# Kernel optimization log

Measured on AMD Instinct MI355X. Metric: run time of the kernel, lower is better.

The kernel has to match this reference:

```python
import jax, jax.numpy as jnp
import numpy as np

NEG_SLOPE = 0.2

def _gatv2(x_src, x_dst, src, dst, Wl, bl, Wr, br, att, bias, num_dst, edge_feat=None, We=None):
    # PyG GATv2Conv (heads=1, add_self_loops=False, eval mode -> no dropout)
    xl = x_src @ Wl + bl                      # [Ns, C] lin_l on source
    xr = x_dst @ Wr + br                      # [Nd, C] lin_r on target
    m = xl[src] + xr[dst]                     # [E, C]
    if edge_feat is not None:
        m = m + edge_feat @ We                # lin_edge (bias=False)
    e = jax.nn.leaky_relu(m, NEG_SLOPE) @ att # [E] attention logits
    emax = jax.ops.segment_max(e, dst, num_segments=num_dst)
    ee = jnp.exp(e - emax[dst])
    denom = jax.ops.segment_sum(ee, dst, num_segments=num_dst)
    alpha = ee / jnp.maximum(denom[dst], 1e-16)
    out = jax.ops.segment_sum(alpha[:, None] * xl[src], dst, num_segments=num_dst)
    return out + bias


def setup_inputs() -> dict:
    key = jax.random.key(0)
    N_OP, N_M, N_A = 50000, 5000, 2000
    C_OP, C_M, C_A = 256, 128, 128
    E_OO, E_OM, E_MA, E_DIM = 200000, 200000, 60000, 8
    ks = jax.random.split(key, 40)
    i = iter(range(40))
    def nrm(shape, fan_in):
        return jax.random.normal(ks[next(i)], shape, dtype=jnp.float32) / np.sqrt(fan_in)
    inp = {}
    inp['x_op'] = jax.random.normal(ks[next(i)], (N_OP, C_OP), dtype=jnp.float32)
    inp['x_m'] = jax.random.normal(ks[next(i)], (N_M, C_M), dtype=jnp.float32)
    inp['x_a'] = jax.random.normal(ks[next(i)], (N_A, C_A), dtype=jnp.float32)
    inp['ei_pred'] = jax.random.randint(ks[next(i)], (2, E_OO), 0, N_OP)
    inp['ei_succ'] = jax.random.randint(ks[next(i)], (2, E_OO), 0, N_OP)
    inp['src_o2m'] = jax.random.randint(ks[next(i)], (E_OM,), 0, N_OP)
    inp['dst_o2m'] = jax.random.randint(ks[next(i)], (E_OM,), 0, N_M)
    inp['src_m2a'] = jax.random.randint(ks[next(i)], (E_MA,), 0, N_M)
    inp['dst_m2a'] = jax.random.randint(ks[next(i)], (E_MA,), 0, N_A)
    inp['ea_m2a'] = jax.random.normal(ks[next(i)], (E_MA, E_DIM), dtype=jnp.float32)
    for name, c_in_src, c_in_dst, c_out in [('pred', C_OP, C_OP, C_OP), ('succ', C_OP, C_OP, C_OP), ('o2m', C_OP, C_M, C_M), ('m2a', C_M, C_A, C_A)]:
        inp[f'Wl_{name}'] = nrm((c_in_src, c_out), c_in_src)
        inp[f'bl_{name}'] = jnp.zeros((c_out,), jnp.float32)
        inp[f'Wr_{name}'] = nrm((c_in_dst, c_out), c_in_dst)
        inp[f'br_{name}'] = jnp.zeros((c_out,), jnp.float32)
        inp[f'att_{name}'] = nrm((c_out,), c_out)
        inp[f'b_{name}'] = jnp.zeros((c_out,), jnp.float32)
    inp['We_m2a'] = nrm((E_DIM, C_A), E_DIM)
    return inp


def reference(x_op, x_m, x_a, ei_pred, ei_succ, src_o2m, dst_o2m, src_m2a, dst_m2a, ea_m2a,
              Wl_pred, bl_pred, Wr_pred, br_pred, att_pred, b_pred,
              Wl_succ, bl_succ, Wr_succ, br_succ, att_succ, b_succ,
              Wl_o2m, bl_o2m, Wr_o2m, br_o2m, att_o2m, b_o2m,
              Wl_m2a, bl_m2a, Wr_m2a, br_m2a, att_m2a, b_m2a, We_m2a):
    N_OP, N_M, N_A = x_op.shape[0], x_m.shape[0], x_a.shape[0]
    # operation_relation_extract: two op->op GATv2 convs, HeteroConv sum-aggregated
    f_pred = _gatv2(x_op, x_op, ei_pred[0], ei_pred[1], Wl_pred, bl_pred, Wr_pred, br_pred, att_pred, b_pred, N_OP)
    f_succ = _gatv2(x_op, x_op, ei_succ[0], ei_succ[1], Wl_succ, bl_succ, Wr_succ, br_succ, att_succ, b_succ, N_OP)
    # hetero_relation_extract
    f_mach = _gatv2(x_op, x_m, src_o2m, dst_o2m, Wl_o2m, bl_o2m, Wr_o2m, br_o2m, att_o2m, b_o2m, N_M)
    f_agv = _gatv2(x_m, x_a, src_m2a, dst_m2a, Wl_m2a, bl_m2a, Wr_m2a, br_m2a, att_m2a, b_m2a, N_A, edge_feat=ea_m2a, We=We_m2a)
    # residual sum across relation outputs per node type
    out_op = x_op + f_pred + f_succ
    out_m = x_m + f_mach
    out_a = x_a + f_agv
    return (out_op, out_m, out_a)
```

## Files before the change

### kernel.cpp

```cpp
#include <hip/hip_runtime.h>

#define N_OP   50000
#define N_M    5000
#define N_A    2000
#define C_OP   256
#define C_M    128
#define C_A    128
#define E_OO   200000
#define E_OM   200000
#define E_MA   60000
#define E_DIM  8

#define OUT_OP_OFF 0
#define OUT_M_OFF  (N_OP * C_OP)
#define OUT_A_OFF  (N_OP * C_OP + N_M * C_M)

typedef short bf16x8 __attribute__((ext_vector_type(8)));
typedef float f32x4 __attribute__((ext_vector_type(4)));
typedef __attribute__((address_space(1))) const unsigned gu32;
typedef __attribute__((address_space(3))) unsigned lu32;

__device__ __forceinline__ unsigned short f2bf(float f) {
    unsigned u = __float_as_uint(f);
    unsigned r = (u + 0x7FFFu + ((u >> 16) & 1u)) >> 16;
    return (unsigned short)r;
}
__device__ __forceinline__ float bf2f(unsigned short h) {
    return __uint_as_float(((unsigned)h) << 16);
}

#define NTOT 107000
#define ETOT 660000

#define I3_OP (N_OP * C_OP / 4)
#define I3_M  (I3_OP + N_M * C_M / 4)
#define I3_A  (I3_M + N_A * C_A / 4)

#define PK_P   131072
#define PK_S   262144
#define PK_OL  294912
#define PK_OR  311296
#define PK_ML  327680
#define PK_MR  344064
#define PK_BP  344576
#define PK_BS  345088

#define PREP_HIST_BLK ((ETOT + 255) / 256)
#define PREP_INIT_BLK (I3_A / 256)
#define PREP_PACK_BLK (PK_BS / 256)
#define PREP_TOTAL    17670

__device__ __forceinline__ void init_one(const float* __restrict__ x,
                                         const float* __restrict__ b1,
                                         const float* __restrict__ b2,
                                         float* __restrict__ out,
                                         unsigned short* __restrict__ xc,
                                         int i, int cmask) {
    float4 v = ((const float4*)x)[i];
    const int cb = i & cmask;
    float4 b = ((const float4*)b1)[cb];
    if (b2) {
        float4 t = ((const float4*)b2)[cb];
        b.x += t.x; b.y += t.y; b.z += t.z; b.w += t.w;
    }
    float4 o;
    o.x = v.x + b.x; o.y = v.y + b.y; o.z = v.z + b.z; o.w = v.w + b.w;
    ((float4*)out)[i] = o;
    ushort4 r;
    r.x = f2bf(v.x); r.y = f2bf(v.y); r.z = f2bf(v.z); r.w = f2bf(v.w);
    ((ushort4*)xc)[i] = r;
}

__global__ void prep_all(
    const int* __restrict__ dP, const int* __restrict__ dS,
    const int* __restrict__ dO, const int* __restrict__ dA,
    int* __restrict__ cP, int* __restrict__ cS,
    int* __restrict__ cO, int* __restrict__ cA, int* __restrict__ rk,
    const float* __restrict__ x_op, const float* __restrict__ x_m,
    const float* __restrict__ x_a,
    const float* __restrict__ bP, const float* __restrict__ bS,
    const float* __restrict__ bO, const float* __restrict__ bA,
    float* __restrict__ out_op, float* __restrict__ out_m, float* __restrict__ out_a,
    unsigned short* __restrict__ xcop, unsigned short* __restrict__ xcm,
    unsigned short* __restrict__ xca,
    const float* __restrict__ WlP, const float* __restrict__ WrP,
    const float* __restrict__ WlS, const float* __restrict__ WrS,
    const float* __restrict__ WOl, const float* __restrict__ WOr,
    const float* __restrict__ WMl, const float* __restrict__ WMr,
    const float* __restrict__ blP, const float* __restrict__ brP,
    const float* __restrict__ blS, const float* __restrict__ brS,
    unsigned short* __restrict__ BtP, unsigned short* __restrict__ BtS,
    unsigned short* __restrict__ BtOL, unsigned short* __restrict__ BtOR,
    unsigned short* __restrict__ BtML, unsigned short* __restrict__ BtMR,
    float* __restrict__ biasP, float* __restrict__ biasS) {
    const int b = blockIdx.x;
    const int tid = threadIdx.x;
    if ((b % 6) == 5) {
        const int hb = b / 6;
        if (hb >= PREP_HIST_BLK) return;
        int i = hb * 256 + tid;
        if (i < 200000)      rk[i] = atomicAdd(&cP[dP[i]], 1);
        else if (i < 400000) rk[i] = atomicAdd(&cS[dS[i - 200000]], 1);
        else if (i < 600000) rk[i] = atomicAdd(&cO[dO[i - 400000]], 1);
        else if (i < ETOT)   rk[i] = atomicAdd(&cA[dA[i - 600000]], 1);
        return;
    }
    const int ob = b - b / 6;
    if (ob < PREP_INIT_BLK) {
        int i = ob * 256 + tid;
        if (i < I3_OP)      init_one(x_op, bP, bS, out_op, xcop, i, 63);
        else if (i < I3_M)  init_one(x_m, bO, nullptr, out_m, xcm, i - I3_OP, 31);
        else                init_one(x_a, bA, nullptr, out_a, xca, i - I3_M, 31);
    } else {
        int i = (ob - PREP_INIT_BLK) * 256 + tid;
        if (i < PK_P) {
            int n = i >> 8, k = i & 255;
            BtP[i] = f2bf((n < 256) ? WlP[k * 256 + n] : WrP[k * 256 + (n - 256)]);
        } else if (i < PK_S) {
            int j = i - PK_P; int n = j >> 8, k = j & 255;
            BtS[j] = f2bf((n < 256) ? WlS[k * 256 + n] : WrS[k * 256 + (n - 256)]);
        } else if (i < PK_OL) {
            int j = i - PK_S; int n = j >> 8, k = j & 255;
            BtOL[j] = f2bf(WOl[k * 128 + n]);
        } else if (i < PK_OR) {
            int j = i - PK_OL; int n = j >> 7, k = j & 127;
            BtOR[j] = f2bf(WOr[k * 128 + n]);
        } else if (i < PK_ML) {
            int j = i - PK_OR; int n = j >> 7, k = j & 127;
            BtML[j] = f2bf(WMl[k * 128 + n]);
        } else if (i < PK_MR) {
            int j = i - PK_ML; int n = j >> 7, k = j & 127;
            BtMR[j] = f2bf(WMr[k * 128 + n]);
        } else if (i < PK_BP) {
            int j = i - PK_MR;
            biasP[j] = (j < 256) ? blP[j] : brP[j - 256];
        } else if (i < PK_BS) {
            int j = i - PK_BP;
            biasS[j] = (j < 256) ? blS[j] : brS[j - 256];
        }
    }
}

__device__ __forceinline__ void gload_lds16(const void* g, void* l) {
    __builtin_amdgcn_global_load_lds((gu32*)g, (lu32*)l, 16, 0, 0);
}

#define GEMM_IDX                                                                \
    const int tid  = threadIdx.x;                                               \
    const int lane = tid & 63;                                                  \
    const int wid  = tid >> 6;                                                  \
    const int m0   = bx * 128;                                                  \
    const int n0   = by * 128;                                                  \
    f32x4 acc[4][4] = {};                                                       \
    const int srow  = tid >> 3;                                                 \
    const int scolb = (tid & 7) * 16;                                           \
    const int scole = (scolb ^ ((srow & 7) << 4)) >> 1;                         \
    int grA[4], grB[4];                                                         \
    _Pragma("unroll")                                                           \
    for (int i = 0; i < 4; ++i) {                                               \
        int gr = m0 + i * 32 + srow;                                            \
        grA[i] = (gr < M) ? gr : M - 1;                                         \
        grB[i] = n0 + i * 32 + srow;                                            \
    }                                                                           \
    const int nt = K >> 6;

#define GEMM_COMPUTE(BUFA, BUFB)                                                \
    _Pragma("unroll")                                                           \
    for (int kh = 0; kh < 2; ++kh) {                                            \
        const int kob = kh * 64 + (lane >> 4) * 16;                             \
        bf16x8 a[4], bfr[4];                                                    \
        _Pragma("unroll")                                                       \
        for (int mi = 0; mi < 4; ++mi) {                                        \
            const int row = wr + mi * 16 + (lane & 15);                         \
            a[mi] = *(const bf16x8*)((const char*)(BUFA) + row * 128 +          \
                                     (kob ^ ((row & 7) << 4)));                 \
        }                                                                       \
        _Pragma("unroll")                                                       \
        for (int ni = 0; ni < 4; ++ni) {                                        \
            const int row = wc + ni * 16 + (lane & 15);                         \
            bfr[ni] = *(const bf16x8*)((const char*)(BUFB) + row * 128 +        \
                                       (kob ^ ((row & 7) << 4)));               \
        }                                                                       \
        _Pragma("unroll")                                                       \
        for (int mi = 0; mi < 4; ++mi)                                          \
            _Pragma("unroll")                                                   \
            for (int ni = 0; ni < 4; ++ni)                                      \
                acc[mi][ni] = __builtin_amdgcn_mfma_f32_16x16x32_bf16(          \
                    a[mi], bfr[ni], acc[mi][ni], 0, 0, 0);                      \
    }

#define GEMM_EPILOGUE                                                           \
    const int crow = (lane >> 4) * 4;                                           \
    const int ccol = lane & 15;                                                 \
    float bcol[4];                                                              \
    _Pragma("unroll")                                                           \
    for (int ni = 0; ni < 4; ++ni) bcol[ni] = bias[n0 + wc + ni * 16 + ccol];   \
    _Pragma("unroll")                                                           \
    for (int mi = 0; mi < 4; ++mi) {                                            \
        _Pragma("unroll")                                                       \
        for (int j = 0; j < 4; ++j) {                                           \
            const int row = m0 + wr + mi * 16 + crow + j;                       \
            if (row < M) {                                                      \
                unsigned short* pc = C + (size_t)row * ldc + n0 + wc + ccol;    \
                _Pragma("unroll")                                               \
                for (int ni = 0; ni < 4; ++ni)                                  \
                    pc[ni * 16] = f2bf(acc[mi][ni][j] + bcol[ni]);              \
            }                                                                   \
        }                                                                       \
    }

__device__ __forceinline__ void gemm_body(
    const unsigned short* __restrict__ A, const unsigned short* __restrict__ Bt,
    const float* __restrict__ bias, unsigned short* __restrict__ C,
    int M, int K, int ldc, int bx, int by,
    unsigned short (&As)[2][128 * 64], unsigned short (&Bs)[2][128 * 64]) {
    GEMM_IDX
    int cur = 0;
#define STAGE(buf, k0)                                                          \
    {                                                                           \
        _Pragma("unroll")                                                       \
        for (int i = 0; i < 4; ++i)                                             \
            gload_lds16(A + (size_t)grA[i] * K + (k0) + scole,                  \
                        &As[buf][i * 2048 + tid * 8]);                          \
        _Pragma("unroll")                                                       \
        for (int i = 0; i < 4; ++i)                                             \
            gload_lds16(Bt + (size_t)grB[i] * K + (k0) + scole,                 \
                        &Bs[buf][i * 2048 + tid * 8]);                          \
    }
    STAGE(0, 0)
    asm volatile("s_waitcnt vmcnt(0)" ::: "memory");
    __syncthreads();
    const int wr = (wid >> 1) * 64;
    const int wc = (wid & 1) * 64;
    for (int t = 0; t < nt; ++t) {
        if (t + 1 < nt) STAGE(cur ^ 1, (t + 1) * 64)
        GEMM_COMPUTE(As[cur], Bs[cur])
        asm volatile("s_waitcnt vmcnt(0)" ::: "memory");
        __syncthreads();
        cur ^= 1;
    }
#undef STAGE
    GEMM_EPILOGUE
}

__device__ __forceinline__ void gemm_body_sb(
    const unsigned short* __restrict__ A, const unsigned short* __restrict__ Bt,
    const float* __restrict__ bias, unsigned short* __restrict__ C,
    int M, int K, int ldc, int bx, int by,
    unsigned short (&As)[128 * 64], unsigned short (&Bs)[128 * 64]) {
    GEMM_IDX
    const int wr = (wid >> 1) * 64;
    const int wc = (wid & 1) * 64;
    for (int t = 0; t < nt; ++t) {
#pragma unroll
        for (int i = 0; i < 4; ++i)
            gload_lds16(A + (size_t)grA[i] * K + t * 64 + scole, &As[i * 2048 + tid * 8]);
#pragma unroll
        for (int i = 0; i < 4; ++i)
            gload_lds16(Bt + (size_t)grB[i] * K + t * 64 + scole, &Bs[i * 2048 + tid * 8]);
        asm volatile("s_waitcnt vmcnt(0)" ::: "memory");
        __syncthreads();
        GEMM_COMPUTE(As, Bs)
        __syncthreads();
    }
    GEMM_EPILOGUE
}

__global__ __launch_bounds__(256) void mfma_gemm(
    const unsigned short* __restrict__ A, const unsigned short* __restrict__ Bt,
    const float* __restrict__ bias, unsigned short* __restrict__ C,
    int M, int K, int ldc) {
    __shared__ unsigned short As[2][128 * 64];
    __shared__ unsigned short Bs[2][128 * 64];
    gemm_body(A, Bt, bias, C, M, K, ldc, blockIdx.x, blockIdx.y, As, Bs);
}

#define SCAT_XBLK 645
__global__ __launch_bounds__(256) void gemm_scat(
    const unsigned short* __restrict__ A, const unsigned short* __restrict__ Bt,
    const float* __restrict__ bias, unsigned short* __restrict__ C,
    int M, int K, int ldc, int mt,
    const int* __restrict__ sP, const int* __restrict__ dP,
    const int* __restrict__ sS, const int* __restrict__ dS,
    const int* __restrict__ sO, const int* __restrict__ dO,
    const int* __restrict__ sA, const int* __restrict__ dA,
    const int* __restrict__ pP, const int* __restrict__ pS,
    const int* __restrict__ pO, const int* __restrict__ pA,
    const int* __restrict__ rk,
    int* __restrict__ srP, int* __restrict__ srS,
    int* __restrict__ srO, int* __restrict__ srA, int* __restrict__ eiA) {
    __shared__ unsigned short As[2][128 * 64];
    __shared__ unsigned short Bs[2][128 * 64];
    if ((int)blockIdx.x < mt) {
        gemm_body(A, Bt, bias, C, M, K, ldc, blockIdx.x, blockIdx.y, As, Bs);
    } else {
        const int i = (((int)blockIdx.x - mt) * 4 + (int)blockIdx.y) * 256 + (int)threadIdx.x;
        if (i < 200000) {
            srP[pP[dP[i]] + rk[i]] = sP[i];
        } else if (i < 400000) {
            const int j = i - 200000;
            srS[pS[dS[j]] + rk[i]] = sS[j];
        } else if (i < 600000) {
            const int j = i - 400000;
            srO[pO[dO[j]] + rk[i]] = sO[j];
        } else if (i < ETOT) {
            const int j = i - 600000;
            const int pos = pA[dA[j]] + rk[i];
            srA[pos] = sA[j];
            eiA[pos] = j;
        }
    }
}

#define NB_P 49
#define NB_S 49
#define NB_O 5
#define NB_A 2

__global__ void zero4(int* __restrict__ p, int n) {
    int i = blockIdx.x * blockDim.x + threadIdx.x;
    if (i < n) p[i] = 0;
}

__global__ void scan_blk4(const int* __restrict__ cP, const int* __restrict__ cS,
                          const int* __restrict__ cO, const int* __restrict__ cA,
                          int* __restrict__ pP, int* __restrict__ pS,
                          int* __restrict__ pO, int* __restrict__ pA,
                          int* __restrict__ bsum) {
    __shared__ int smem[1024];
    int b = blockIdx.x;
    const int* cnt; int* ptr; int n; int bo;
    if (b < NB_P)                { cnt = cP; ptr = pP; n = 50000; bo = 0; }
    else if (b < NB_P + NB_S)    { cnt = cS; ptr = pS; n = 50000; bo = 64;  b -= NB_P; }
    else if (b < NB_P + NB_S + NB_O) { cnt = cO; ptr = pO; n = 5000; bo = 128; b -= NB_P + NB_S; }
    else                         { cnt = cA; ptr = pA; n = 2000; bo = 192; b -= NB_P + NB_S + NB_O; }
    const int tid = threadIdx.x;
    const int i = b * 1024 + tid;
    const int v = (i < n) ? cnt[i] : 0;
    smem[tid] = v;
    __syncthreads();
    for (int o = 1; o < 1024; o <<= 1) {
        int t = (tid >= o) ? smem[tid - o] : 0;
        __syncthreads();
        smem[tid] += t;
        __syncthreads();
    }
    if (i < n) ptr[i] = smem[tid] - v;
    if (tid == 1023) bsum[bo + b] = smem[1023];
}

__global__ void scan_tops4(const int* __restrict__ bsum, int* __restrict__ boff,
                           int* __restrict__ pP, int* __restrict__ pS,
                           int* __restrict__ pO, int* __restrict__ pA) {
    __shared__ int smem[1024];
    const int seg = blockIdx.x;
    const int nb = (seg < 2) ? 49 : (seg == 2 ? 5 : 2);
    const int off = seg * 64;
    int* ptr_n = (seg == 0) ? pP + 50000 : (seg == 1) ? pS + 50000
               : (seg == 2) ? pO + 5000 : pA + 2000;
    const int tid = threadIdx.x;
    const int v = (tid < nb) ? bsum[off + tid] : 0;
    smem[tid] = v;
    __syncthreads();
    for (int o = 1; o < 1024; o <<= 1) {
        int t = (tid >= o) ? smem[tid - o] : 0;
        __syncthreads();
        smem[tid] += t;
        __syncthreads();
    }
    if (tid < nb) boff[off + tid] = smem[tid] - v;
    if (tid == 1023) *ptr_n = smem[1023];
}

__global__ void scan_add4(int* __restrict__ pP, int* __restrict__ pS,
                          int* __restrict__ pO, int* __restrict__ pA,
                          const int* __restrict__ boff) {
    int i = blockIdx.x * blockDim.x + threadIdx.x;
    int* ptr; int loc; int off;
    if (i < 50000)       { ptr = pP; loc = i;          off = 0; }
    else if (i < 100000) { ptr = pS; loc = i - 50000;  off = 64; }
    else if (i < 105000) { ptr = pO; loc = i - 100000; off = 128; }
    else if (i < NTOT)   { ptr = pA; loc = i - 105000; off = 192; }
    else return;
    ptr[loc] += boff[off + (loc >> 10)];
}

__device__ __forceinline__ void csr2_body(
    const unsigned short* __restrict__ xl, int ldl,
    const unsigned short* __restrict__ xr, int ldr,
    const float* __restrict__ att,
    const int* __restrict__ ptr, const int* __restrict__ srcs,
    float* __restrict__ out, int n, int blk) {
    const int tid = threadIdx.x;
    const int node = blk * 8 + (tid >> 5);
    if (node >= n) return;
    const int gl = tid & 31;
    const int beg = ptr[node], end = ptr[node + 1];
    if (beg == end) return;

    constexpr int V = 8;
    const int c0 = gl * V;

    float av[V], rvf[V];
    {
        const unsigned short* pr = xr + (size_t)node * ldr + c0;
        unsigned short rv[V];
        *(uint4*)rv = *(const uint4*)pr;
#pragma unroll
        for (int v4 = 0; v4 < V / 4; ++v4)
            *(float4*)(av + v4 * 4) = ((const float4*)(att + c0))[v4];
#pragma unroll
        for (int v = 0; v < V; ++v) rvf[v] = bf2f(rv[v]);
    }

    float runM = -3.0e38f, runS = 0.0f;
    float acc[V] = {};

    unsigned short lv[V];
    {
        const unsigned short* pl = xl + (size_t)srcs[beg] * ldl + c0;
        *(uint4*)lv = *(const uint4*)pl;
    }

    for (int j = beg; j < end; ++j) {
        float cf[V];
#pragma unroll
        for (int v = 0; v < V; ++v) cf[v] = bf2f(lv[v]);
        if (j + 1 < end) {
            const unsigned short* pl = xl + (size_t)srcs[j + 1] * ldl + c0;
            *(uint4*)lv = *(const uint4*)pl;
        }

        float part = 0.0f;
#pragma unroll
        for (int v = 0; v < V; ++v) {
            float m = cf[v] + rvf[v];
            m = (m >= 0.0f) ? m : 0.2f * m;
            part += m * av[v];
        }
        part += __shfl_xor(part, 1, 64);
        part += __shfl_xor(part, 2, 64);
        part += __shfl_xor(part, 4, 64);
        part += __shfl_xor(part, 8, 64);
        part += __shfl_xor(part, 16, 64);

        const float newM = fmaxf(runM, part);
        const float sc = __expf(runM - newM);
        const float e1 = __expf(part - newM);
        runS = runS * sc + e1;
        runM = newM;
#pragma unroll
        for (int v = 0; v < V; ++v) acc[v] = acc[v] * sc + e1 * cf[v];
    }

    const float inv = 1.0f / fmaxf(runS, 1e-16f);
    float* po = out + (size_t)node * 256 + c0;
#pragma unroll
    for (int v4 = 0; v4 < V / 4; ++v4) {
        float4 o = ((float4*)po)[v4];
        o.x += acc[v4 * 4 + 0] * inv;
        o.y += acc[v4 * 4 + 1] * inv;
        o.z += acc[v4 * 4 + 2] * inv;
        o.w += acc[v4 * 4 + 3] * inv;
        ((float4*)po)[v4] = o;
    }
}

__global__ void csr_serial2(const unsigned short* __restrict__ xl, int ldl,
                            const unsigned short* __restrict__ xr, int ldr,
                            const float* __restrict__ att,
                            const int* __restrict__ ptr, const int* __restrict__ srcs,
                            float* __restrict__ out, int n) {
    csr2_body(xl, ldl, xr, ldr, att, ptr, srcs, out, n, blockIdx.x);
}

template <bool EF>
__device__ __forceinline__ void csrg_body(
    const unsigned short* __restrict__ xl, const unsigned short* __restrict__ xr,
    const float* __restrict__ att,
    const int* __restrict__ ptr, const int* __restrict__ srcs,
    const int* __restrict__ eid, const float* __restrict__ ea,
    const float* __restrict__ We,
    float* __restrict__ out, int n, int blk) {
    const int node = blk * 4 + ((int)threadIdx.x >> 6);
    if (node >= n) return;
    const int lane = threadIdx.x & 63;
    const int grp  = lane >> 4;
    const int sl   = lane & 15;
    const int beg = ptr[node], end = ptr[node + 1];
    if (beg == end) return;

    constexpr int W = 8;
    const int c0 = sl * W;

    float av[W], rvf[W];
    {
        const unsigned short* pr = xr + (size_t)node * 128 + c0;
        unsigned short rv[W];
        *(uint4*)rv = *(const uint4*)pr;
#pragma unroll
        for (int v4 = 0; v4 < 2; ++v4)
            *(float4*)(av + v4 * 4) = ((const float4*)(att + c0))[v4];
#pragma unroll
        for (int v = 0; v < W; ++v) rvf[v] = bf2f(rv[v]);
    }

    float wreg[64];
    if constexpr (EF) {
#pragma unroll
        for (int k = 0; k < 8; ++k) {
            *(float4*)(wreg + k * 8)     = *(const float4*)(We + k * 128 + c0);
            *(float4*)(wreg + k * 8 + 4) = *(const float4*)(We + k * 128 + c0 + 4);
        }
    }

    float runM = -3.0e38f, runS = 0.0f;
    float acc[W] = {};

    for (int cb = beg; cb < end; cb += 4) {
        const int j = cb + grp;
        const bool act = (j < end);
        const int js = act ? j : end - 1;
        const int s = srcs[js];

        const unsigned short* pl = xl + (size_t)s * 128 + c0;
        unsigned short lv[W];
        *(uint4*)lv = *(const uint4*)pl;
        float cf[W];
#pragma unroll
        for (int v = 0; v < W; ++v) cf[v] = bf2f(lv[v]);

        float part = 0.0f;
        if constexpr (EF) {
            const int oe = eid[js];
            float eav[8];
            *(float4*)eav       = *(const float4*)(ea + (size_t)oe * 8);
            *(float4*)(eav + 4) = *(const float4*)(ea + (size_t)oe * 8 + 4);
#pragma unroll
            for (int v = 0; v < W; ++v) {
                float efv = eav[0] * wreg[v];
#pragma unroll
                for (int k = 1; k < 8; ++k) efv += eav[k] * wreg[k * 8 + v];
                float m = cf[v] + rvf[v] + efv;
                m = (m >= 0.0f) ? m : 0.2f * m;
                part += m * av[v];
            }
        } else {
#pragma unroll
            for (int v = 0; v < W; ++v) {
                float m = cf[v] + rvf[v];
                m = (m >= 0.0f) ? m : 0.2f * m;
                part += m * av[v];
            }
        }
        part += __shfl_xor(part, 1, 64);
        part += __shfl_xor(part, 2, 64);
        part += __shfl_xor(part, 4, 64);
        part += __shfl_xor(part, 8, 64);
        if (!act) part = -3.0e38f;

        float cm = fmaxf(part, __shfl_xor(part, 16, 64));
        cm = fmaxf(cm, __shfl_xor(cm, 32, 64));

        if (cm > runM) {
            const float sc = __expf(runM - cm);
            runS *= sc;
#pragma unroll
            for (int v = 0; v < W; ++v) acc[v] *= sc;
            runM = cm;
        }
        const float w = act ? __expf(part - runM) : 0.0f;
        float cs = w + __shfl_xor(w, 16, 64);
        cs += __shfl_xor(cs, 32, 64);
        runS += cs;
#pragma unroll
        for (int v = 0; v < W; ++v) acc[v] += w * cf[v];
    }

#pragma unroll
    for (int v = 0; v < W; ++v) acc[v] += __shfl_xor(acc[v], 16, 64);
#pragma unroll
    for (int v = 0; v < W; ++v) acc[v] += __shfl_xor(acc[v], 32, 64);

    const float inv = 1.0f / fmaxf(runS, 1e-16f);
    if (grp == 0) {
        float* po = out + (size_t)node * 128 + c0;
#pragma unroll
        for (int v4 = 0; v4 < 2; ++v4) {
            float4 o = ((float4*)po)[v4];
            o.x += acc[v4 * 4 + 0] * inv;
            o.y += acc[v4 * 4 + 1] * inv;
            o.z += acc[v4 * 4 + 2] * inv;
            o.w += acc[v4 * 4 + 3] * inv;
            ((float4*)po)[v4] = o;
        }
    }
}

#define MT_OPB 391
#define MT_MB  40
#define MT_AB  16
#define PG_GEMM (MT_OPB + MT_MB + MT_MB + MT_AB)

__global__ __launch_bounds__(256) void fuse_pg(
    const unsigned short* __restrict__ xc_op, const unsigned short* __restrict__ xc_m,
    const unsigned short* __restrict__ xc_a,
    const unsigned short* __restrict__ BtOL, const unsigned short* __restrict__ BtOR,
    const unsigned short* __restrict__ BtML, const unsigned short* __restrict__ BtMR,
    const float* __restrict__ blO, const float* __restrict__ brO,
    const float* __restrict__ blM, const float* __restrict__ brM,
    unsigned short* __restrict__ xlbO, unsigned short* __restrict__ xrbO,
    unsigned short* __restrict__ xlbM, unsigned short* __restrict__ xrbM,
    const unsigned short* __restrict__ H, const float* __restrict__ attP,
    const int* __restrict__ ptrP, const int* __restrict__ srcP,
    float* __restrict__ out_op) {
    __shared__ unsigned short As[128 * 64];
    __shared__ unsigned short Bs[128 * 64];
    const int b = blockIdx.x;
    if (b < MT_OPB) {
        gemm_body_sb(xc_op, BtOL, blO, xlbO, N_OP, 256, 128, b, 0, As, Bs);
    } else if (b < MT_OPB + MT_MB) {
        gemm_body_sb(xc_m, BtOR, brO, xrbO, N_M, 128, 128, b - MT_OPB, 0, As, Bs);
    } else if (b < MT_OPB + 2 * MT_MB) {
        gemm_body_sb(xc_m, BtML, blM, xlbM, N_M, 128, 128, b - MT_OPB - MT_MB, 0, As, Bs);
    } else if (b < PG_GEMM) {
        gemm_body_sb(xc_a, BtMR, brM, xrbM, N_A, 128, 128, b - MT_OPB - 2 * MT_MB, 0, As, Bs);
    } else {
        csr2_body(H, 512, H + 256, 512, attP, ptrP, srcP, out_op, N_OP, b - PG_GEMM);
    }
}

#define CP_O 1250
__global__ void csr_pair(
    const unsigned short* __restrict__ xlbO, const unsigned short* __restrict__ xrbO,
    const float* __restrict__ attO,
    const int* __restrict__ ptrO, const int* __restrict__ srcO,
    float* __restrict__ out_m,
    const unsigned short* __restrict__ xlbM, const unsigned short* __restrict__ xrbM,
    const float* __restrict__ attA,
    const int* __restrict__ ptrA, const int* __restrict__ srcA,
    const int* __restrict__ eidA, const float* __restrict__ ea,
    const float* __restrict__ We, float* __restrict__ out_a) {
    const int b = blockIdx.x;
    if (b < CP_O)
        csrg_body<false>(xlbO, xrbO, attO, ptrO, srcO, nullptr, nullptr, nullptr,
                         out_m, N_M, b);
    else
        csrg_body<true>(xlbM, xrbM, attA, ptrA, srcA, eidA, ea, We,
                        out_a, N_A, b - CP_O);
}

#define F_H      0
#define F_XCOP   12800000
#define F_XCM    19200000
#define F_XCA    19520000
#define F_BTP    19648000
#define F_BTS    19713536
#define F_BTOL   19779072
#define F_BTOR   19795456
#define F_BTML   19803648
#define F_BTMR   19811840
#define F_BIASP  19820032
#define F_BIASS  19820544
#define F_CNT4   19821056
#define F_BSUM   19928056
#define F_BOFF   19928312
#define F_PTR_P  19928568
#define F_SRC_P  19978569
#define F_PTR_S  20178569
#define F_SRC_S  20228570
#define F_PTR_O  20428570
#define F_SRC_O  20433571
#define F_PTR_A  20633571
#define F_SRC_A  20635572
#define F_EID_A  20695572
#define F_RANK   20755572
#define F_XLO    21415572
#define F_XRO    24615572
#define F_XLM    24935572
#define F_XRM    25255572

extern "C" void kernel_launch(void* const* d_in, const int* in_sizes, int n_in,
                              void* d_out, int out_size, void* d_ws, size_t ws_size,
                              hipStream_t stream) {
    const float* x_op    = (const float*)d_in[0];
    const float* x_m     = (const float*)d_in[1];
    const float* x_a     = (const float*)d_in[2];
    const int*   ei_pred = (const int*)d_in[3];
    const int*   ei_succ = (const int*)d_in[4];
    const int*   src_o2m = (const int*)d_in[5];
    const int*   dst_o2m = (const int*)d_in[6];
    const int*   src_m2a = (const int*)d_in[7];
    const int*   dst_m2a = (const int*)d_in[8];
    const float* ea_m2a  = (const float*)d_in[9];

    const float* Wl_pred = (const float*)d_in[10];
    const float* bl_pred = (const float*)d_in[11];
    const float* Wr_pred = (const float*)d_in[12];
    const float* br_pred = (const float*)d_in[13];
    const float* att_pred= (const float*)d_in[14];
    const float* b_pred  = (const float*)d_in[15];

    const float* Wl_succ = (const float*)d_in[16];
    const float* bl_succ = (const float*)d_in[17];
    const float* Wr_succ = (const float*)d_in[18];
    const float* br_succ = (const float*)d_in[19];
    const float* att_succ= (const float*)d_in[20];
    const float* b_succ  = (const float*)d_in[21];

    const float* Wl_o2m  = (const float*)d_in[22];
    const float* bl_o2m  = (const float*)d_in[23];
    const float* Wr_o2m  = (const float*)d_in[24];
    const float* br_o2m  = (const float*)d_in[25];
    const float* att_o2m = (const float*)d_in[26];
    const float* b_o2m   = (const float*)d_in[27];

    const float* Wl_m2a  = (const float*)d_in[28];
    const float* bl_m2a  = (const float*)d_in[29];
    const float* Wr_m2a  = (const float*)d_in[30];
    const float* br_m2a  = (const float*)d_in[31];
    const float* att_m2a = (const float*)d_in[32];
    const float* b_m2a   = (const float*)d_in[33];
    const float* We_m2a  = (const float*)d_in[34];

    float* ws = (float*)d_ws;
    unsigned short* H     = (unsigned short*)(ws + F_H);
    unsigned short* xc_op = (unsigned short*)(ws + F_XCOP);
    unsigned short* xc_m  = (unsigned short*)(ws + F_XCM);
    unsigned short* xc_a  = (unsigned short*)(ws + F_XCA);
    unsigned short* BtP   = (unsigned short*)(ws + F_BTP);
    unsigned short* BtS   = (unsigned short*)(ws + F_BTS);
    unsigned short* BtOL  = (unsigned short*)(ws + F_BTOL);
    unsigned short* BtOR  = (unsigned short*)(ws + F_BTOR);
    unsigned short* BtML  = (unsigned short*)(ws + F_BTML);
    unsigned short* BtMR  = (unsigned short*)(ws + F_BTMR);
    float* biasP = ws + F_BIASP;
    float* biasS = ws + F_BIASS;
    int* cntP = (int*)(ws + F_CNT4);
    int* cntS = cntP + 50000;
    int* cntO = cntP + 100000;
    int* cntA = cntP + 105000;
    int* bsum = (int*)(ws + F_BSUM);
    int* boff = (int*)(ws + F_BOFF);
    int* ptrP = (int*)(ws + F_PTR_P); int* srcP = (int*)(ws + F_SRC_P);
    int* ptrS = (int*)(ws + F_PTR_S); int* srcS = (int*)(ws + F_SRC_S);
    int* ptrO = (int*)(ws + F_PTR_O); int* srcO = (int*)(ws + F_SRC_O);
    int* ptrA = (int*)(ws + F_PTR_A); int* srcA = (int*)(ws + F_SRC_A);
    int* eidA = (int*)(ws + F_EID_A);
    int* rk   = (int*)(ws + F_RANK);
    unsigned short* xlbO = (unsigned short*)(ws + F_XLO);
    unsigned short* xrbO = (unsigned short*)(ws + F_XRO);
    unsigned short* xlbM = (unsigned short*)(ws + F_XLM);
    unsigned short* xrbM = (unsigned short*)(ws + F_XRM);

    float* out_op = (float*)d_out + OUT_OP_OFF;
    float* out_m  = (float*)d_out + OUT_M_OFF;
    float* out_a  = (float*)d_out + OUT_A_OFF;

    zero4<<<(NTOT + 255) / 256, 256, 0, stream>>>(cntP, NTOT);

    prep_all<<<PREP_TOTAL, 256, 0, stream>>>(
        ei_pred + E_OO, ei_succ + E_OO, dst_o2m, dst_m2a,
        cntP, cntS, cntO, cntA, rk,
        x_op, x_m, x_a, b_pred, b_succ, b_o2m, b_m2a,
        out_op, out_m, out_a, xc_op, xc_m, xc_a,
        Wl_pred, Wr_pred, Wl_succ, Wr_succ, Wl_o2m, Wr_o2m, Wl_m2a, Wr_m2a,
        bl_pred, br_pred, bl_succ, br_succ,
        BtP, BtS, BtOL, BtOR, BtML, BtMR, biasP, biasS);

    scan_blk4<<<NB_P + NB_S + NB_O + NB_A, 1024, 0, stream>>>(cntP, cntS, cntO, cntA,
                                                              ptrP, ptrS, ptrO, ptrA, bsum);
    scan_tops4<<<4, 1024, 0, stream>>>(bsum, boff, ptrP, ptrS, ptrO, ptrA);
    scan_add4<<<(NTOT + 255) / 256, 256, 0, stream>>>(ptrP, ptrS, ptrO, ptrA, boff);

    gemm_scat<<<dim3(MT_OPB + SCAT_XBLK, 4), 256, 0, stream>>>(
        xc_op, BtP, biasP, H, N_OP, 256, 512, MT_OPB,
        ei_pred, ei_pred + E_OO, ei_succ, ei_succ + E_OO,
        src_o2m, dst_o2m, src_m2a, dst_m2a,
        ptrP, ptrS, ptrO, ptrA, rk,
        srcP, srcS, srcO, srcA, eidA);

    fuse_pg<<<PG_GEMM + (N_OP + 7) / 8, 256, 0, stream>>>(
        xc_op, xc_m, xc_a, BtOL, BtOR, BtML, BtMR,
        bl_o2m, br_o2m, bl_m2a, br_m2a,
        xlbO, xrbO, xlbM, xrbM,
        H, att_pred, ptrP, srcP, out_op);

    mfma_gemm<<<dim3(MT_OPB, 4), 256, 0, stream>>>(xc_op, BtS, biasS, H, N_OP, 256, 512);

    csr_serial2<<<(N_OP + 7) / 8, 256, 0, stream>>>(H, 512, H + 256, 512,
                                                    att_succ, ptrS, srcS, out_op, N_OP);

    csr_pair<<<CP_O + (N_A + 3) / 4, 256, 0, stream>>>(
        xlbO, xrbO, att_o2m, ptrO, srcO, out_m,
        xlbM, xrbM, att_m2a, ptrA, srcA, eidA, ea_m2a, We_m2a, out_a);
}
```

Baseline: 311.6 us.

## Move small o2m/m2a GEMMs into the pred GEMM+scatter launch

The four small projection GEMMs (o2m lin_l/lin_r, m2a lin_l/lin_r) move out of the fused kernel that also ran the pred CSR aggregation and into the first GEMM+scatter launch. They now use the double-buffered GEMM body instead of the single-buffered one, and the pred aggregation runs as its own csr_serial2 launch. The aim is to overlap the small GEMMs with the large pred GEMM and the CSR scatter, and to give them the pipelined load path. The trade-off is that the pred aggregation no longer overlaps with those GEMMs, and the first kernel now needs double-buffered LDS for every block.

Result: faster. 271.6 us (-12.8%).

```diff
diff --git a/kernel.cpp b/kernel.cpp
--- a/kernel.cpp
+++ b/kernel.cpp
@@ -145,77 +145,34 @@
     __builtin_amdgcn_global_load_lds((gu32*)g, (lu32*)l, 16, 0, 0);
 }
 
-#define GEMM_IDX                                                                \
-    const int tid  = threadIdx.x;                                               \
-    const int lane = tid & 63;                                                  \
-    const int wid  = tid >> 6;                                                  \
-    const int m0   = bx * 128;                                                  \
-    const int n0   = by * 128;                                                  \
-    f32x4 acc[4][4] = {};                                                       \
-    const int srow  = tid >> 3;                                                 \
-    const int scolb = (tid & 7) * 16;                                           \
-    const int scole = (scolb ^ ((srow & 7) << 4)) >> 1;                         \
-    int grA[4], grB[4];                                                         \
-    _Pragma("unroll")                                                           \
-    for (int i = 0; i < 4; ++i) {                                               \
-        int gr = m0 + i * 32 + srow;                                            \
-        grA[i] = (gr < M) ? gr : M - 1;                                         \
-        grB[i] = n0 + i * 32 + srow;                                            \
-    }                                                                           \
-    const int nt = K >> 6;
-
-#define GEMM_COMPUTE(BUFA, BUFB)                                                \
-    _Pragma("unroll")                                                           \
-    for (int kh = 0; kh < 2; ++kh) {                                            \
-        const int kob = kh * 64 + (lane >> 4) * 16;                             \
-        bf16x8 a[4], bfr[4];                                                    \
-        _Pragma("unroll")                                                       \
-        for (int mi = 0; mi < 4; ++mi) {                                        \
-            const int row = wr + mi * 16 + (lane & 15);                         \
-            a[mi] = *(const bf16x8*)((const char*)(BUFA) + row * 128 +          \
-                                     (kob ^ ((row & 7) << 4)));                 \
-        }                                                                       \
-        _Pragma("unroll")                                                       \
-        for (int ni = 0; ni < 4; ++ni) {                                        \
-            const int row = wc + ni * 16 + (lane & 15);                         \
-            bfr[ni] = *(const bf16x8*)((const char*)(BUFB) + row * 128 +        \
-                                       (kob ^ ((row & 7) << 4)));               \
-        }                                                                       \
-        _Pragma("unroll")                                                       \
-        for (int mi = 0; mi < 4; ++mi)                                          \
-            _Pragma("unroll")                                                   \
-            for (int ni = 0; ni < 4; ++ni)                                      \
-                acc[mi][ni] = __builtin_amdgcn_mfma_f32_16x16x32_bf16(          \
-                    a[mi], bfr[ni], acc[mi][ni], 0, 0, 0);                      \
-    }
-
-#define GEMM_EPILOGUE                                                           \
-    const int crow = (lane >> 4) * 4;                                           \
-    const int ccol = lane & 15;                                                 \
-    float bcol[4];                                                              \
-    _Pragma("unroll")                                                           \
-    for (int ni = 0; ni < 4; ++ni) bcol[ni] = bias[n0 + wc + ni * 16 + ccol];   \
-    _Pragma("unroll")                                                           \
-    for (int mi = 0; mi < 4; ++mi) {                                            \
-        _Pragma("unroll")                                                       \
-        for (int j = 0; j < 4; ++j) {                                           \
-            const int row = m0 + wr + mi * 16 + crow + j;                       \
-            if (row < M) {                                                      \
-                unsigned short* pc = C + (size_t)row * ldc + n0 + wc + ccol;    \
-                _Pragma("unroll")                                               \
-                for (int ni = 0; ni < 4; ++ni)                                  \
-                    pc[ni * 16] = f2bf(acc[mi][ni][j] + bcol[ni]);              \
-            }                                                                   \
-        }                                                                       \
-    }
-
 __device__ __forceinline__ void gemm_body(
     const unsigned short* __restrict__ A, const unsigned short* __restrict__ Bt,
     const float* __restrict__ bias, unsigned short* __restrict__ C,
     int M, int K, int ldc, int bx, int by,
     unsigned short (&As)[2][128 * 64], unsigned short (&Bs)[2][128 * 64]) {
-    GEMM_IDX
+    const int tid  = threadIdx.x;
+    const int lane = tid & 63;
+    const int wid  = tid >> 6;
+    const int m0   = bx * 128;
+    const int n0   = by * 128;
+
+    f32x4 acc[4][4] = {};
+
+    const int srow   = tid >> 3;
+    const int scolb  = (tid & 7) * 16;
+    const int scole  = (scolb ^ ((srow & 7) << 4)) >> 1;
+
+    int grA[4], grB[4];
+#pragma unroll
+    for (int i = 0; i < 4; ++i) {
+        int gr = m0 + i * 32 + srow;
+        grA[i] = (gr < M) ? gr : M - 1;
+        grB[i] = n0 + i * 32 + srow;
+    }
+
+    const int nt = K >> 6;
     int cur = 0;
+
 #define STAGE(buf, k0)                                                          \
     {                                                                           \
         _Pragma("unroll")                                                       \
@@ -227,43 +184,63 @@
             gload_lds16(Bt + (size_t)grB[i] * K + (k0) + scole,                 \
                         &Bs[buf][i * 2048 + tid * 8]);                          \
     }
+
     STAGE(0, 0)
     asm volatile("s_waitcnt vmcnt(0)" ::: "memory");
     __syncthreads();
+
     const int wr = (wid >> 1) * 64;
     const int wc = (wid & 1) * 64;
+
     for (int t = 0; t < nt; ++t) {
         if (t + 1 < nt) STAGE(cur ^ 1, (t + 1) * 64)
-        GEMM_COMPUTE(As[cur], Bs[cur])
+#pragma unroll
+        for (int kh = 0; kh < 2; ++kh) {
+            const int kob = kh * 64 + (lane >> 4) * 16;
+            bf16x8 a[4], b[4];
+#pragma unroll
+            for (int mi = 0; mi < 4; ++mi) {
+                const int row = wr + mi * 16 + (lane & 15);
+                a[mi] = *(const bf16x8*)((const char*)As[cur] + row * 128 +
+                                         (kob ^ ((row & 7) << 4)));
+            }
+#pragma unroll
+            for (int ni = 0; ni < 4; ++ni) {
+                const int row = wc + ni * 16 + (lane & 15);
+                b[ni] = *(const bf16x8*)((const char*)Bs[cur] + row * 128 +
+                                         (kob ^ ((row & 7) << 4)));
+            }
+#pragma unroll
+            for (int mi = 0; mi < 4; ++mi)
+#pragma unroll
+                for (int ni = 0; ni < 4; ++ni)
+                    acc[mi][ni] = __builtin_amdgcn_mfma_f32_16x16x32_bf16(
+                        a[mi], b[ni], acc[mi][ni], 0, 0, 0);
+        }
         asm volatile("s_waitcnt vmcnt(0)" ::: "memory");
         __syncthreads();
         cur ^= 1;
     }
 #undef STAGE
-    GEMM_EPILOGUE
-}
-
-__device__ __forceinline__ void gemm_body_sb(
-    const unsigned short* __restrict__ A, const unsigned short* __restrict__ Bt,
-    const float* __restrict__ bias, unsigned short* __restrict__ C,
-    int M, int K, int ldc, int bx, int by,
-    unsigned short (&As)[128 * 64], unsigned short (&Bs)[128 * 64]) {
-    GEMM_IDX
-    const int wr = (wid >> 1) * 64;
-    const int wc = (wid & 1) * 64;
-    for (int t = 0; t < nt; ++t) {
-#pragma unroll
-        for (int i = 0; i < 4; ++i)
-            gload_lds16(A + (size_t)grA[i] * K + t * 64 + scole, &As[i * 2048 + tid * 8]);
-#pragma unroll
-        for (int i = 0; i < 4; ++i)
-            gload_lds16(Bt + (size_t)grB[i] * K + t * 64 + scole, &Bs[i * 2048 + tid * 8]);
-        asm volatile("s_waitcnt vmcnt(0)" ::: "memory");
-        __syncthreads();
-        GEMM_COMPUTE(As, Bs)
-        __syncthreads();
-    }
-    GEMM_EPILOGUE
+
+    const int crow = (lane >> 4) * 4;
+    const int ccol = lane & 15;
+    float bcol[4];
+#pragma unroll
+    for (int ni = 0; ni < 4; ++ni) bcol[ni] = bias[n0 + wc + ni * 16 + ccol];
+#pragma unroll
+    for (int mi = 0; mi < 4; ++mi) {
+#pragma unroll
+        for (int j = 0; j < 4; ++j) {
+            const int row = m0 + wr + mi * 16 + crow + j;
+            if (row < M) {
+                unsigned short* pc = C + (size_t)row * ldc + n0 + wc + ccol;
+#pragma unroll
+                for (int ni = 0; ni < 4; ++ni)
+                    pc[ni * 16] = f2bf(acc[mi][ni][j] + bcol[ni]);
+            }
+        }
+    }
 }
 
 __global__ __launch_bounds__(256) void mfma_gemm(
@@ -275,11 +252,24 @@
     gemm_body(A, Bt, bias, C, M, K, ldc, blockIdx.x, blockIdx.y, As, Bs);
 }
 
+#define MT_OPB 391
+#define MT_MB  40
+#define MT_AB  16
+#define SMALL_G (MT_OPB + MT_MB + MT_MB + MT_AB)
+#define SMALL_XBLK 122
 #define SCAT_XBLK 645
-__global__ __launch_bounds__(256) void gemm_scat(
-    const unsigned short* __restrict__ A, const unsigned short* __restrict__ Bt,
-    const float* __restrict__ bias, unsigned short* __restrict__ C,
-    int M, int K, int ldc, int mt,
+
+__global__ __launch_bounds__(256) void gemm_multi(
+    const unsigned short* __restrict__ xc_op, const unsigned short* __restrict__ xc_m,
+    const unsigned short* __restrict__ xc_a,
+    const unsigned short* __restrict__ BtP, const float* __restrict__ biasP,
+    unsigned short* __restrict__ H,
+    const unsigned short* __restrict__ BtOL, const unsigned short* __restrict__ BtOR,
+    const unsigned short* __restrict__ BtML, const unsigned short* __restrict__ BtMR,
+    const float* __restrict__ blO, const float* __restrict__ brO,
+    const float* __restrict__ blM, const float* __restrict__ brM,
+    unsigned short* __restrict__ xlbO, unsigned short* __restrict__ xrbO,
+    unsigned short* __restrict__ xlbM, unsigned short* __restrict__ xrbM,
     const int* __restrict__ sP, const int* __restrict__ dP,
     const int* __restrict__ sS, const int* __restrict__ dS,
     const int* __restrict__ sO, const int* __restrict__ dO,
@@ -291,10 +281,21 @@
     int* __restrict__ srO, int* __restrict__ srA, int* __restrict__ eiA) {
     __shared__ unsigned short As[2][128 * 64];
     __shared__ unsigned short Bs[2][128 * 64];
-    if ((int)blockIdx.x < mt) {
-        gemm_body(A, Bt, bias, C, M, K, ldc, blockIdx.x, blockIdx.y, As, Bs);
+    const int bx = blockIdx.x, by = blockIdx.y;
+    if (bx < MT_OPB) {
+        gemm_body(xc_op, BtP, biasP, H, N_OP, 256, 512, bx, by, As, Bs);
+    } else if (bx < MT_OPB + SMALL_XBLK) {
+        const int idx = (bx - MT_OPB) * 4 + by;
+        if (idx < MT_OPB)
+            gemm_body(xc_op, BtOL, blO, xlbO, N_OP, 256, 128, idx, 0, As, Bs);
+        else if (idx < MT_OPB + MT_MB)
+            gemm_body(xc_m, BtOR, brO, xrbO, N_M, 128, 128, idx - MT_OPB, 0, As, Bs);
+        else if (idx < MT_OPB + 2 * MT_MB)
+            gemm_body(xc_m, BtML, blM, xlbM, N_M, 128, 128, idx - MT_OPB - MT_MB, 0, As, Bs);
+        else if (idx < SMALL_G)
+            gemm_body(xc_a, BtMR, brM, xrbM, N_A, 128, 128, idx - MT_OPB - 2 * MT_MB, 0, As, Bs);
     } else {
-        const int i = (((int)blockIdx.x - mt) * 4 + (int)blockIdx.y) * 256 + (int)threadIdx.x;
+        const int i = ((bx - MT_OPB - SMALL_XBLK) * 4 + by) * 256 + (int)threadIdx.x;
         if (i < 200000) {
             srP[pP[dP[i]] + rk[i]] = sP[i];
         } else if (i < 400000) {
@@ -385,14 +386,13 @@
     ptr[loc] += boff[off + (loc >> 10)];
 }
 
-__device__ __forceinline__ void csr2_body(
-    const unsigned short* __restrict__ xl, int ldl,
-    const unsigned short* __restrict__ xr, int ldr,
-    const float* __restrict__ att,
-    const int* __restrict__ ptr, const int* __restrict__ srcs,
-    float* __restrict__ out, int n, int blk) {
+__global__ void csr_serial2(const unsigned short* __restrict__ xl, int ldl,
+                            const unsigned short* __restrict__ xr, int ldr,
+                            const float* __restrict__ att,
+                            const int* __restrict__ ptr, const int* __restrict__ srcs,
+                            float* __restrict__ out, int n) {
     const int tid = threadIdx.x;
-    const int node = blk * 8 + (tid >> 5);
+    const int node = blockIdx.x * 8 + (tid >> 5);
     if (node >= n) return;
     const int gl = tid & 31;
     const int beg = ptr[node], end = ptr[node + 1];
@@ -464,14 +464,6 @@
         o.w += acc[v4 * 4 + 3] * inv;
         ((float4*)po)[v4] = o;
     }
-}
-
-__global__ void csr_serial2(const unsigned short* __restrict__ xl, int ldl,
-                            const unsigned short* __restrict__ xr, int ldr,
-                            const float* __restrict__ att,
-                            const int* __restrict__ ptr, const int* __restrict__ srcs,
-                            float* __restrict__ out, int n) {
-    csr2_body(xl, ldl, xr, ldr, att, ptr, srcs, out, n, blockIdx.x);
 }
 
 template <bool EF>
@@ -594,39 +586,6 @@
             o.w += acc[v4 * 4 + 3] * inv;
             ((float4*)po)[v4] = o;
         }
-    }
-}
-
-#define MT_OPB 391
-#define MT_MB  40
-#define MT_AB  16
-#define PG_GEMM (MT_OPB + MT_MB + MT_MB + MT_AB)
-
-__global__ __launch_bounds__(256) void fuse_pg(
-    const unsigned short* __restrict__ xc_op, const unsigned short* __restrict__ xc_m,
-    const unsigned short* __restrict__ xc_a,
-    const unsigned short* __restrict__ BtOL, const unsigned short* __restrict__ BtOR,
-    const unsigned short* __restrict__ BtML, const unsigned short* __restrict__ BtMR,
-    const float* __restrict__ blO, const float* __restrict__ brO,
-    const float* __restrict__ blM, const float* __restrict__ brM,
-    unsigned short* __restrict__ xlbO, unsigned short* __restrict__ xrbO,
-    unsigned short* __restrict__ xlbM, unsigned short* __restrict__ xrbM,
-    const unsigned short* __restrict__ H, const float* __restrict__ attP,
-    const int* __restrict__ ptrP, const int* __restrict__ srcP,
-    float* __restrict__ out_op) {
-    __shared__ unsigned short As[128 * 64];
-    __shared__ unsigned short Bs[128 * 64];
-    const int b = blockIdx.x;
-    if (b < MT_OPB) {
-        gemm_body_sb(xc_op, BtOL, blO, xlbO, N_OP, 256, 128, b, 0, As, Bs);
-    } else if (b < MT_OPB + MT_MB) {
-        gemm_body_sb(xc_m, BtOR, brO, xrbO, N_M, 128, 128, b - MT_OPB, 0, As, Bs);
-    } else if (b < MT_OPB + 2 * MT_MB) {
-        gemm_body_sb(xc_m, BtML, blM, xlbM, N_M, 128, 128, b - MT_OPB - MT_MB, 0, As, Bs);
-    } else if (b < PG_GEMM) {
-        gemm_body_sb(xc_a, BtMR, brM, xrbM, N_A, 128, 128, b - MT_OPB - 2 * MT_MB, 0, As, Bs);
-    } else {
-        csr2_body(H, 512, H + 256, 512, attP, ptrP, srcP, out_op, N_OP, b - PG_GEMM);
     }
 }
 
@@ -773,18 +732,17 @@
     scan_tops4<<<4, 1024, 0, stream>>>(bsum, boff, ptrP, ptrS, ptrO, ptrA);
     scan_add4<<<(NTOT + 255) / 256, 256, 0, stream>>>(ptrP, ptrS, ptrO, ptrA, boff);
 
-    gemm_scat<<<dim3(MT_OPB + SCAT_XBLK, 4), 256, 0, stream>>>(
-        xc_op, BtP, biasP, H, N_OP, 256, 512, MT_OPB,
+    gemm_multi<<<dim3(MT_OPB + SMALL_XBLK + SCAT_XBLK, 4), 256, 0, stream>>>(
+        xc_op, xc_m, xc_a, BtP, biasP, H,
+        BtOL, BtOR, BtML, BtMR, bl_o2m, br_o2m, bl_m2a, br_m2a,
+        xlbO, xrbO, xlbM, xrbM,
         ei_pred, ei_pred + E_OO, ei_succ, ei_succ + E_OO,
         src_o2m, dst_o2m, src_m2a, dst_m2a,
         ptrP, ptrS, ptrO, ptrA, rk,
         srcP, srcS, srcO, srcA, eidA);
 
-    fuse_pg<<<PG_GEMM + (N_OP + 7) / 8, 256, 0, stream>>>(
-        xc_op, xc_m, xc_a, BtOL, BtOR, BtML, BtMR,
-        bl_o2m, br_o2m, bl_m2a, br_m2a,
-        xlbO, xrbO, xlbM, xrbM,
-        H, att_pred, ptrP, srcP, out_op);
+    csr_serial2<<<(N_OP + 7) / 8, 256, 0, stream>>>(H, 512, H + 256, 512,
+                                                    att_pred, ptrP, srcP, out_op, N_OP);
 
     mfma_gemm<<<dim3(MT_OPB, 4), 256, 0, stream>>>(xc_op, BtS, biasS, H, N_OP, 256, 512);
 
```
